# Performance work log

Measured on AMD Instinct MI355X. Metric: run time of the kernel, lower is better.

## Reference

```python
import jax, jax.numpy as jnp
import numpy as np

T_THRESH = 1.0  # t_thresh init arg


def _step_fn(x):
    # Heaviside forward (gradient handled separately in bwd module)
    return (x > 0).astype(x.dtype)


def setup_inputs() -> dict:
    key = jax.random.key(0)
    k1, = jax.random.split(key, 1)
    x = jax.random.normal(k1, (64, 500, 1024), dtype=jnp.float32)
    w_input = jnp.asarray(1.0, dtype=jnp.float32)
    w_leak = jnp.asarray(0.1, dtype=jnp.float32)
    return {"x": x, "w_input": w_input, "w_leak": w_leak}


def reference(x, w_input, w_leak):
    # Leaky integrate-and-fire over time axis (axis=1).
    # Vm_t = relu(w_i * x_t + (1 - w_l) * Vm_{t-1} * step(t_thresh - Vm_{t-1}))
    # spike_t = step(Vm_t - t_thresh)
    def step(Vm, xt):  # Vm, xt: [B, C]
        forget = _step_fn(T_THRESH - Vm)  # reset if Vm crossed threshold
        Vm = jax.nn.relu(w_input * xt + (1.0 - w_leak) * Vm * forget)
        spike = _step_fn(Vm - T_THRESH)
        return Vm, spike

    Vm0 = jnp.zeros_like(x[:, 0])  # [B, C]
    xt = jnp.swapaxes(x, 0, 1)  # [T, B, C]
    _, spikes = jax.lax.scan(step, Vm0, xt)
    return jnp.swapaxes(spikes, 0, 1)  # [B, T, C]
```

## Files before the change

kernel.cpp:

```cpp
#include <hip/hip_runtime.h>


#define LIF_B 64
#define LIF_T 500
#define LIF_C 1024
#define LIF_TC 25
#define LIF_NCH (LIF_T / LIF_TC)
#define LIF_BC 256

#define GLOBAL_AS(p) ((__attribute__((address_space(1))) const void*)(uintptr_t)(p))
#define LDS_AS(p)    ((__attribute__((address_space(3))) void*)(uintptr_t)(p))

__global__ __launch_bounds__(256) void lif_kernel(
    const float* __restrict__ x,
    const float* __restrict__ w_input_p,
    const float* __restrict__ w_leak_p,
    float* __restrict__ out) {

  __shared__ float lds[2][LIF_TC * LIF_BC];

  const int b     = blockIdx.x >> 2;
  const int cbase = (blockIdx.x & 3) << 8;
  const int tidx  = threadIdx.x;
  const int wave  = tidx >> 6;
  const int lane  = tidx & 63;

  const float wi = w_input_p[0];
  const float kl = __fsub_rn(1.0f, w_leak_p[0]);

  const float* xblk = x   + (size_t)b * LIF_T * LIF_C + cbase;
  float*       oblk = out + (size_t)b * LIF_T * LIF_C + cbase;

  auto stage = [&](int k, int p) {
    const float* src0 = xblk + (size_t)k * LIF_TC * LIF_C;
#pragma unroll
    for (int r0 = 0; r0 < LIF_TC; r0 += 4) {
      const int r = r0 + wave;
      if (r < LIF_TC) {
        const float* g = src0 + (size_t)r * LIF_C + lane * 4;
        float* l = &lds[p][r * LIF_BC];
        __builtin_amdgcn_global_load_lds(GLOBAL_AS(g), LDS_AS(l), 16, 0, 0);
      }
    }
  };

  stage(0, 0);

  float Vm = 0.0f;

  for (int k = 0; k < LIF_NCH; ++k) {
    const int p = k & 1;
    __syncthreads();
    if (k + 1 < LIF_NCH) stage(k + 1, p ^ 1);

    float* orow = oblk + (size_t)k * LIF_TC * LIF_C + tidx;
#pragma unroll
    for (int r = 0; r < LIF_TC; ++r) {
      const float xt  = lds[p][r * LIF_BC + tidx];
      const float acc = (Vm < 1.0f) ? __fmul_rn(kl, Vm) : 0.0f;
      const float v   = __fadd_rn(__fmul_rn(wi, xt), acc);
      Vm = fmaxf(v, 0.0f);
      orow[(size_t)r * LIF_C] = (Vm > 1.0f) ? 1.0f : 0.0f;
    }
  }
}

extern "C" void kernel_launch(void* const* d_in, const int* in_sizes, int n_in,
                              void* d_out, int out_size, void* d_ws, size_t ws_size,
                              hipStream_t stream) {
  const float* x  = (const float*)d_in[0];
  const float* wi = (const float*)d_in[1];
  const float* wl = (const float*)d_in[2];
  float* out = (float*)d_out;

  const int grid = LIF_B * (LIF_C / LIF_BC);
  lif_kernel<<<grid, 256, 0, stream>>>(x, wi, wl, out);
}
```

Baseline: 231.6 us.

## Use single-wave blocks with a deep per-timestep async LDS ring buffer

Each block becomes one 64-thread wave, and each lane handles four adjacent channels as a float4. Input rows are prefetched one timestep at a time into a 32-slot LDS ring with up to 31 asynchronous global-to-LDS loads in flight. Readiness is tracked with manual s_waitcnt vmcnt instead of per-chunk __syncthreads. This removes block-wide barriers and uses vectorized 16-byte stores, but it cuts resident waves per CU to one. The fixed vmcnt threshold also counts the interleaved stores, so the effective prefetch depth is smaller than the ring size.

Result: slower. 413.3 us (+78.5%).

```diff
diff --git a/kernel.cpp b/kernel.cpp
--- a/kernel.cpp
+++ b/kernel.cpp
@@ -4,64 +4,66 @@
 #define LIF_B 64
 #define LIF_T 500
 #define LIF_C 1024
-#define LIF_TC 25
-#define LIF_NCH (LIF_T / LIF_TC)
-#define LIF_BC 256
+#define DEPTH 31
+#define RING  32
 
 #define GLOBAL_AS(p) ((__attribute__((address_space(1))) const void*)(uintptr_t)(p))
 #define LDS_AS(p)    ((__attribute__((address_space(3))) void*)(uintptr_t)(p))
 
-__global__ __launch_bounds__(256) void lif_kernel(
+__global__ __launch_bounds__(64) void lif_kernel(
     const float* __restrict__ x,
     const float* __restrict__ w_input_p,
     const float* __restrict__ w_leak_p,
     float* __restrict__ out) {
 
-  __shared__ float lds[2][LIF_TC * LIF_BC];
+  __shared__ float4 ring[RING][64];
 
   const int b     = blockIdx.x >> 2;
   const int cbase = (blockIdx.x & 3) << 8;
-  const int tidx  = threadIdx.x;
-  const int wave  = tidx >> 6;
-  const int lane  = tidx & 63;
+  const int lane  = threadIdx.x;
 
   const float wi = w_input_p[0];
   const float kl = __fsub_rn(1.0f, w_leak_p[0]);
 
-  const float* xblk = x   + (size_t)b * LIF_T * LIF_C + cbase;
-  float*       oblk = out + (size_t)b * LIF_T * LIF_C + cbase;
+  const float* xs = x   + (size_t)b * LIF_T * LIF_C + cbase + lane * 4;
+  float*       os = out + (size_t)b * LIF_T * LIF_C + cbase + lane * 4;
 
-  auto stage = [&](int k, int p) {
-    const float* src0 = xblk + (size_t)k * LIF_TC * LIF_C;
-#pragma unroll
-    for (int r0 = 0; r0 < LIF_TC; r0 += 4) {
-      const int r = r0 + wave;
-      if (r < LIF_TC) {
-        const float* g = src0 + (size_t)r * LIF_C + lane * 4;
-        float* l = &lds[p][r * LIF_BC];
-        __builtin_amdgcn_global_load_lds(GLOBAL_AS(g), LDS_AS(l), 16, 0, 0);
-      }
-    }
+  auto stage = [&](int t) {
+    __builtin_amdgcn_global_load_lds(GLOBAL_AS(xs + (size_t)t * LIF_C),
+                                     LDS_AS(&ring[t & (RING - 1)][0]),
+                                     16, 0, 0);
   };
 
-  stage(0, 0);
+#pragma unroll
+  for (int t = 0; t < DEPTH; ++t) stage(t);
+  asm volatile("s_waitcnt vmcnt(30)" ::: "memory");
 
-  float Vm = 0.0f;
+  float V0 = 0.0f, V1 = 0.0f, V2 = 0.0f, V3 = 0.0f;
 
-  for (int k = 0; k < LIF_NCH; ++k) {
-    const int p = k & 1;
-    __syncthreads();
-    if (k + 1 < LIF_NCH) stage(k + 1, p ^ 1);
+  for (int t = 0; t < LIF_T; ++t) {
+    asm volatile("s_waitcnt vmcnt(31)" ::: "memory");
 
-    float* orow = oblk + (size_t)k * LIF_TC * LIF_C + tidx;
-#pragma unroll
-    for (int r = 0; r < LIF_TC; ++r) {
-      const float xt  = lds[p][r * LIF_BC + tidx];
-      const float acc = (Vm < 1.0f) ? __fmul_rn(kl, Vm) : 0.0f;
-      const float v   = __fadd_rn(__fmul_rn(wi, xt), acc);
-      Vm = fmaxf(v, 0.0f);
-      orow[(size_t)r * LIF_C] = (Vm > 1.0f) ? 1.0f : 0.0f;
+    const float4 xt = ring[t & (RING - 1)][lane];
+
+    float4 sp;
+    {
+      const float a0 = (V0 < 1.0f) ? __fmul_rn(kl, V0) : 0.0f;
+      V0 = fmaxf(__fadd_rn(__fmul_rn(wi, xt.x), a0), 0.0f);
+      sp.x = (V0 > 1.0f) ? 1.0f : 0.0f;
+      const float a1 = (V1 < 1.0f) ? __fmul_rn(kl, V1) : 0.0f;
+      V1 = fmaxf(__fadd_rn(__fmul_rn(wi, xt.y), a1), 0.0f);
+      sp.y = (V1 > 1.0f) ? 1.0f : 0.0f;
+      const float a2 = (V2 < 1.0f) ? __fmul_rn(kl, V2) : 0.0f;
+      V2 = fmaxf(__fadd_rn(__fmul_rn(wi, xt.z), a2), 0.0f);
+      sp.z = (V2 > 1.0f) ? 1.0f : 0.0f;
+      const float a3 = (V3 < 1.0f) ? __fmul_rn(kl, V3) : 0.0f;
+      V3 = fmaxf(__fadd_rn(__fmul_rn(wi, xt.w), a3), 0.0f);
+      sp.w = (V3 > 1.0f) ? 1.0f : 0.0f;
     }
+
+    if (t + DEPTH < LIF_T) stage(t + DEPTH);
+
+    *(float4*)(os + (size_t)t * LIF_C) = sp;
   }
 }
 
@@ -73,6 +75,6 @@
   const float* wl = (const float*)d_in[2];
   float* out = (float*)d_out;
 
-  const int grid = LIF_B * (LIF_C / LIF_BC);
-  lif_kernel<<<grid, 256, 0, stream>>>(x, wi, wl, out);
+  const int grid = LIF_B * 4;
+  lif_kernel<<<grid, 64, 0, stream>>>(x, wi, wl, out);
 }
```
